# Kernel optimization log

Hardware: AMD Instinct MI355X
Metric: run time of the kernel (lower is better)

The kernel has to match this reference:

```python
import jax, jax.numpy as jnp
import numpy as np

NUM_HEADS = 6

def setup_inputs() -> dict:
    key = jax.random.key(0)
    k1, k2, k3, k4 = jax.random.split(key, 4)
    B, T, C = 128, 256, 384
    s = 1.0 / np.sqrt(C)
    return {
        'x': jax.random.normal(k1, (B, T, C), dtype=jnp.float32),
        'Wq': jax.random.normal(k2, (C, C), dtype=jnp.float32) * s,
        'Wk': jax.random.normal(k3, (C, C), dtype=jnp.float32) * s,
        'Wv': jax.random.normal(k4, (C, C), dtype=jnp.float32) * s,
    }

def reference(x, Wq, Wk, Wv):
    B, T, C = x.shape
    H = NUM_HEADS
    d = C // H
    # projections (bias-free Linear), split into heads
    q = (x @ Wq).reshape(B, T, H, d)
    k = (x @ Wk).reshape(B, T, H, d)
    v = (x @ Wv).reshape(B, T, H, d)
    # NOTE: original scales by 1/sqrt(C), not 1/sqrt(head_dim)
    scale = 1.0 / jnp.sqrt(jnp.asarray(C, dtype=x.dtype))
    att = jnp.einsum('bqhd,bkhd->bhqk', q, k) * scale  # [B,H,T,T]
    causal = jnp.tril(jnp.ones((T, T), dtype=bool))
    att = jnp.where(causal, att, -jnp.inf)
    att = jax.nn.softmax(att, axis=-1)
    # dropout is identity in eval/deterministic mode
    out = jnp.einsum('bhqk,bkhd->bqhd', att, v)  # [B,T,H,d]
    return out.reshape(B, T, C)
```

## Files before the change

### kernel.cpp

```cpp
#include <hip/hip_runtime.h>


typedef unsigned short u16;
typedef float f32x4 __attribute__((ext_vector_type(4)));
typedef short s16x8 __attribute__((ext_vector_type(8)));

static constexpr int BB = 128;
static constexpr int TT = 256;
static constexpr int CC = 384;
static constexpr int HH = 6;
static constexpr int DD = 64;
static constexpr int MM = BB * TT;

static constexpr size_t QOFF  = 0;
static constexpr size_t KOFF  = (size_t)MM * CC;
static constexpr size_t VOFF  = (size_t)2 * MM * CC;
static constexpr size_t WTOFF = (size_t)3 * MM * CC;
static constexpr size_t XOFF  = WTOFF + (size_t)3 * CC * CC;

static constexpr float CSC = 0.07362242194579907f;

__device__ __forceinline__ u16 f2bf(float f) {
  unsigned u = __float_as_uint(f);
  u += 0x7fffu + ((u >> 16) & 1u);
  return (u16)(u >> 16);
}

__global__ void xconv(const float* __restrict__ X, u16* __restrict__ ws) {
  size_t i = (size_t)(blockIdx.x * 256 + threadIdx.x) * 8;
  f32x4 a0 = *(const f32x4*)(X + i);
  f32x4 a1 = *(const f32x4*)(X + i + 4);
  s16x8 ab;
#pragma unroll
  for (int j = 0; j < 4; ++j) { ab[j] = (short)f2bf(a0[j]); ab[4 + j] = (short)f2bf(a1[j]); }
  *(s16x8*)(ws + XOFF + i) = ab;
}

__global__ void wtrans(const float* __restrict__ Wq, const float* __restrict__ Wk,
                       const float* __restrict__ Wv, u16* __restrict__ ws) {
  const float* W = (blockIdx.y == 0) ? Wq : (blockIdx.y == 1) ? Wk : Wv;
  const float sc = (blockIdx.y == 0) ? CSC : 1.0f;
  u16* WT = ws + WTOFF + (size_t)blockIdx.y * CC * CC;
  int i = blockIdx.x * 256 + threadIdx.x;
  int k = i / CC, n = i % CC;
  WT[(size_t)n * CC + k] = f2bf(W[i] * sc);
}

__global__ __launch_bounds__(256) void gemm_qkv(u16* __restrict__ ws) {
  const u16* Xbf = ws + XOFF;
  const u16* WT3 = ws + WTOFF;

  __shared__ u16 As[128][72];
  __shared__ u16 Bs[128][72];

  const int tid = threadIdx.x;
  const int lane = tid & 63;
  const int w = tid >> 6;
  const int quad = lane >> 4;
  const int col = lane & 15;
  const int m0 = blockIdx.x * 128;
  const int n0 = blockIdx.y * 128;
  const int z = blockIdx.y / 3;
  const int wm = (w >> 1) * 64;
  const int wn = (w & 1) * 64;

  f32x4 acc[4][4] = {};

  for (int kt = 0; kt < 6; ++kt) {
    if (kt) __syncthreads();
#pragma unroll
    for (int i = 0; i < 4; ++i) {
      int c = i * 256 + tid;
      int row = c >> 3, c8 = (c & 7) * 8;
      *(uint4*)(&As[row][c8]) =
          *(const uint4*)(Xbf + (size_t)(m0 + row) * CC + kt * 64 + c8);
      *(uint4*)(&Bs[row][c8]) =
          *(const uint4*)(WT3 + (size_t)(n0 + row) * CC + kt * 64 + c8);
    }
    __syncthreads();

    s16x8 af[4][2], bf[4][2];
#pragma unroll
    for (int mt = 0; mt < 4; ++mt)
#pragma unroll
      for (int ks = 0; ks < 2; ++ks)
        af[mt][ks] = *(const s16x8*)(&As[wm + mt * 16 + col][ks * 32 + quad * 8]);
#pragma unroll
    for (int nt = 0; nt < 4; ++nt)
#pragma unroll
      for (int ks = 0; ks < 2; ++ks)
        bf[nt][ks] = *(const s16x8*)(&Bs[wn + nt * 16 + col][ks * 32 + quad * 8]);

#pragma unroll
    for (int ks = 0; ks < 2; ++ks)
#pragma unroll
      for (int mt = 0; mt < 4; ++mt)
#pragma unroll
        for (int nt = 0; nt < 4; ++nt)
          acc[mt][nt] = __builtin_amdgcn_mfma_f32_16x16x32_bf16(
              af[mt][ks], bf[nt][ks], acc[mt][nt], 0, 0, 0);
  }

  if (z == 2) {
#pragma unroll
    for (int mt = 0; mt < 4; ++mt)
#pragma unroll
      for (int nt = 0; nt < 4; ++nt) {
        int tok = m0 + wm + mt * 16 + quad * 4;
        int bb = tok >> 8, t = tok & 255;
        int ng = (n0 - 2 * CC) + wn + nt * 16 + col;
        int hh = ng >> 6, d = ng & 63;
        uint2 pk;
        pk.x = (unsigned)f2bf(acc[mt][nt][0]) | ((unsigned)f2bf(acc[mt][nt][1]) << 16);
        pk.y = (unsigned)f2bf(acc[mt][nt][2]) | ((unsigned)f2bf(acc[mt][nt][3]) << 16);
        *(uint2*)(ws + VOFF + (((size_t)(bb * HH + hh) * DD + d) * TT + t)) = pk;
      }
  } else {
    u16* Y = ws + (size_t)z * MM * CC;
    const int nz = n0 - z * CC;
#pragma unroll
    for (int mt = 0; mt < 4; ++mt)
#pragma unroll
      for (int nt = 0; nt < 4; ++nt) {
        int mg = m0 + wm + mt * 16 + quad * 4;
        int ng = nz + wn + nt * 16 + col;
#pragma unroll
        for (int r = 0; r < 4; ++r)
          Y[(size_t)(mg + r) * CC + ng] = f2bf(acc[mt][nt][r]);
      }
  }
}

__global__ __launch_bounds__(128) void attn(const u16* __restrict__ ws,
                                            float* __restrict__ out) {
  const int bx = blockIdx.x;
  const int qt = 3 - (bx / 768);
  const int bh = bx % 768;
  const int b = bh / HH;
  const int h = bh % HH;

  __shared__ u16 Ps[2][16][72];

  const int tid = threadIdx.x;
  const int lane = tid & 63;
  const int w = tid >> 6;
  const int quad = lane >> 4;
  const int col = lane & 15;
  const int q0 = qt * 64 + w * 32;

  const u16* Qg = ws + QOFF;
  const u16* Kg = ws + KOFF;
  const u16* VTg = ws + VOFF;

  s16x8 qf[2][2];
#pragma unroll
  for (int mt = 0; mt < 2; ++mt)
#pragma unroll
    for (int ks = 0; ks < 2; ++ks)
      qf[mt][ks] = *(const s16x8*)(Qg + (size_t)(b * TT + q0 + mt * 16 + col) * CC +
                                   h * DD + ks * 32 + quad * 8);

  f32x4 o[2][4] = {};
  float mst[2] = {-1.0e30f, -1.0e30f}, lst[2] = {0.0f, 0.0f};

  for (int kt = 0; kt <= qt; ++kt) {
    s16x8 kf[4][2], vf[4][2];
#pragma unroll
    for (int nt = 0; nt < 4; ++nt)
#pragma unroll
      for (int ks = 0; ks < 2; ++ks) {
        kf[nt][ks] = *(const s16x8*)(Kg + (size_t)(b * TT + kt * 64 + nt * 16 + col) * CC +
                                     h * DD + ks * 32 + quad * 8);
        vf[nt][ks] = *(const s16x8*)(VTg + ((size_t)(bh * DD + nt * 16 + col) * TT +
                                     kt * 64 + ks * 32 + quad * 8));
      }

#pragma unroll
    for (int mt = 0; mt < 2; ++mt) {
      f32x4 s[4] = {};
#pragma unroll
      for (int ks = 0; ks < 2; ++ks)
#pragma unroll
        for (int nt = 0; nt < 4; ++nt)
          s[nt] = __builtin_amdgcn_mfma_f32_16x16x32_bf16(kf[nt][ks], qf[mt][ks],
                                                          s[nt], 0, 0, 0);

      float rmax = -1.0e30f;
#pragma unroll
      for (int nt = 0; nt < 4; ++nt)
#pragma unroll
        for (int r = 0; r < 4; ++r) {
          float t = s[nt][r];
          if (kt == qt && (nt * 16 + quad * 4 + r) > (w * 32 + mt * 16 + col)) t = -1.0e30f;
          s[nt][r] = t;
          rmax = fmaxf(rmax, t);
        }
      rmax = fmaxf(rmax, __shfl_xor(rmax, 16));
      rmax = fmaxf(rmax, __shfl_xor(rmax, 32));

      float mn = fmaxf(mst[mt], rmax);
      float alpha = exp2f(mst[mt] - mn);
      mst[mt] = mn;

      float lsum = 0.0f;
      unsigned pk[4][2];
#pragma unroll
      for (int nt = 0; nt < 4; ++nt) {
        float p0 = exp2f(s[nt][0] - mn), p1 = exp2f(s[nt][1] - mn);
        float p2 = exp2f(s[nt][2] - mn), p3 = exp2f(s[nt][3] - mn);
        lsum += (p0 + p1) + (p2 + p3);
        pk[nt][0] = (unsigned)f2bf(p0) | ((unsigned)f2bf(p1) << 16);
        pk[nt][1] = (unsigned)f2bf(p2) | ((unsigned)f2bf(p3) << 16);
      }
      lst[mt] = lst[mt] * alpha + lsum;

#pragma unroll
      for (int dt = 0; dt < 4; ++dt)
#pragma unroll
        for (int r = 0; r < 4; ++r) o[mt][dt][r] *= alpha;

      asm volatile("s_waitcnt lgkmcnt(0)" ::: "memory");
#pragma unroll
      for (int nt = 0; nt < 4; ++nt)
        *(uint2*)(&Ps[w][col][nt * 16 + quad * 4]) = make_uint2(pk[nt][0], pk[nt][1]);
      asm volatile("s_waitcnt lgkmcnt(0)" ::: "memory");

      s16x8 pf[2];
#pragma unroll
      for (int ks = 0; ks < 2; ++ks)
        pf[ks] = *(const s16x8*)(&Ps[w][col][ks * 32 + quad * 8]);

#pragma unroll
      for (int ks = 0; ks < 2; ++ks)
#pragma unroll
        for (int dt = 0; dt < 4; ++dt)
          o[mt][dt] = __builtin_amdgcn_mfma_f32_16x16x32_bf16(vf[dt][ks], pf[ks],
                                                              o[mt][dt], 0, 0, 0);
    }
  }

#pragma unroll
  for (int mt = 0; mt < 2; ++mt) {
    float l = lst[mt];
    l += __shfl_xor(l, 16);
    l += __shfl_xor(l, 32);
    float inv = 1.0f / l;
    int q = q0 + mt * 16 + col;
#pragma unroll
    for (int dt = 0; dt < 4; ++dt) {
      f32x4 res;
#pragma unroll
      for (int r = 0; r < 4; ++r) res[r] = o[mt][dt][r] * inv;
      *(f32x4*)(out + (size_t)(b * TT + q) * CC + h * DD + dt * 16 + quad * 4) = res;
    }
  }
}

extern "C" void kernel_launch(void* const* d_in, const int* in_sizes, int n_in,
                              void* d_out, int out_size, void* d_ws, size_t ws_size,
                              hipStream_t stream) {
  const float* x  = (const float*)d_in[0];
  const float* wq = (const float*)d_in[1];
  const float* wk = (const float*)d_in[2];
  const float* wv = (const float*)d_in[3];
  u16* ws  = (u16*)d_ws;
  float* out = (float*)d_out;

  xconv<<<dim3(MM * CC / (256 * 8)), 256, 0, stream>>>(x, ws);
  wtrans<<<dim3(CC * CC / 256, 3), 256, 0, stream>>>(wq, wk, wv, ws);
  gemm_qkv<<<dim3(MM / 128, 9), 256, 0, stream>>>(ws);
  attn<<<dim3(BB * HH * 4), 128, 0, stream>>>(ws, out);
}
```

Measured before the change: 184.0 us.

## Merge prep kernels and load GEMM tiles via direct global-to-LDS with XOR swizzle

Folds the x conversion and weight transpose kernels into a single prep launch to save one kernel launch. In the QKV GEMM, the tile staging now uses global_load_lds to copy straight from global memory into shared memory, skipping the register round trip. The unpadded LDS tiles use an XOR swizzle on 16-byte chunks to avoid bank conflicts. This depends on the lane-to-LDS address mapping of the builtin matching the swizzled layout.

After: 180.3 us. -2.0%, faster.

```diff
diff --git a/kernel.cpp b/kernel.cpp
--- a/kernel.cpp
+++ b/kernel.cpp
@@ -26,32 +26,42 @@
   return (u16)(u >> 16);
 }
 
-__global__ void xconv(const float* __restrict__ X, u16* __restrict__ ws) {
-  size_t i = (size_t)(blockIdx.x * 256 + threadIdx.x) * 8;
-  f32x4 a0 = *(const f32x4*)(X + i);
-  f32x4 a1 = *(const f32x4*)(X + i + 4);
-  s16x8 ab;
-#pragma unroll
-  for (int j = 0; j < 4; ++j) { ab[j] = (short)f2bf(a0[j]); ab[4 + j] = (short)f2bf(a1[j]); }
-  *(s16x8*)(ws + XOFF + i) = ab;
-}
-
-__global__ void wtrans(const float* __restrict__ Wq, const float* __restrict__ Wk,
-                       const float* __restrict__ Wv, u16* __restrict__ ws) {
-  const float* W = (blockIdx.y == 0) ? Wq : (blockIdx.y == 1) ? Wk : Wv;
-  const float sc = (blockIdx.y == 0) ? CSC : 1.0f;
-  u16* WT = ws + WTOFF + (size_t)blockIdx.y * CC * CC;
-  int i = blockIdx.x * 256 + threadIdx.x;
-  int k = i / CC, n = i % CC;
-  WT[(size_t)n * CC + k] = f2bf(W[i] * sc);
+__device__ __forceinline__ void g2l16(const u16* g, u16* l) {
+  __builtin_amdgcn_global_load_lds(
+      (const __attribute__((address_space(1))) u16*)g,
+      (__attribute__((address_space(3))) u16*)l, 16, 0, 0);
+}
+
+__global__ void prep(const float* __restrict__ X, const float* __restrict__ Wq,
+                     const float* __restrict__ Wk, const float* __restrict__ Wv,
+                     u16* __restrict__ ws) {
+  int bx = blockIdx.x;
+  if (bx < 6144) {
+    size_t i = (size_t)(bx * 256 + threadIdx.x) * 8;
+    f32x4 a0 = *(const f32x4*)(X + i);
+    f32x4 a1 = *(const f32x4*)(X + i + 4);
+    s16x8 ab;
+#pragma unroll
+    for (int j = 0; j < 4; ++j) { ab[j] = (short)f2bf(a0[j]); ab[4 + j] = (short)f2bf(a1[j]); }
+    *(s16x8*)(ws + XOFF + i) = ab;
+  } else {
+    int j = bx - 6144;
+    int z = j / 576;
+    const float* W = (z == 0) ? Wq : (z == 1) ? Wk : Wv;
+    const float sc = (z == 0) ? CSC : 1.0f;
+    u16* WT = ws + WTOFF + (size_t)z * CC * CC;
+    int i = (j % 576) * 256 + threadIdx.x;
+    int k = i / CC, n = i % CC;
+    WT[(size_t)n * CC + k] = f2bf(W[i] * sc);
+  }
 }
 
 __global__ __launch_bounds__(256) void gemm_qkv(u16* __restrict__ ws) {
   const u16* Xbf = ws + XOFF;
   const u16* WT3 = ws + WTOFF;
 
-  __shared__ u16 As[128][72];
-  __shared__ u16 Bs[128][72];
+  __shared__ u16 As[128][64];
+  __shared__ u16 Bs[128][64];
 
   const int tid = threadIdx.x;
   const int lane = tid & 63;
@@ -64,18 +74,18 @@
   const int wm = (w >> 1) * 64;
   const int wn = (w & 1) * 64;
 
+  const int rl = lane >> 3;
+  const int gb = (lane & 7) ^ rl;
+
   f32x4 acc[4][4] = {};
 
   for (int kt = 0; kt < 6; ++kt) {
     if (kt) __syncthreads();
 #pragma unroll
     for (int i = 0; i < 4; ++i) {
-      int c = i * 256 + tid;
-      int row = c >> 3, c8 = (c & 7) * 8;
-      *(uint4*)(&As[row][c8]) =
-          *(const uint4*)(Xbf + (size_t)(m0 + row) * CC + kt * 64 + c8);
-      *(uint4*)(&Bs[row][c8]) =
-          *(const uint4*)(WT3 + (size_t)(n0 + row) * CC + kt * 64 + c8);
+      int r0 = (w * 4 + i) * 8;
+      g2l16(Xbf + (size_t)(m0 + r0 + rl) * CC + kt * 64 + gb * 8, &As[r0][0]);
+      g2l16(WT3 + (size_t)(n0 + r0 + rl) * CC + kt * 64 + gb * 8, &Bs[r0][0]);
     }
     __syncthreads();
 
@@ -84,12 +94,14 @@
     for (int mt = 0; mt < 4; ++mt)
 #pragma unroll
       for (int ks = 0; ks < 2; ++ks)
-        af[mt][ks] = *(const s16x8*)(&As[wm + mt * 16 + col][ks * 32 + quad * 8]);
+        af[mt][ks] = *(const s16x8*)(&As[wm + mt * 16 + col]
+                                        [(((ks * 4 + quad) ^ (col & 7)) * 8)]);
 #pragma unroll
     for (int nt = 0; nt < 4; ++nt)
 #pragma unroll
       for (int ks = 0; ks < 2; ++ks)
-        bf[nt][ks] = *(const s16x8*)(&Bs[wn + nt * 16 + col][ks * 32 + quad * 8]);
+        bf[nt][ks] = *(const s16x8*)(&Bs[wn + nt * 16 + col]
+                                        [(((ks * 4 + quad) ^ (col & 7)) * 8)]);
 
 #pragma unroll
     for (int ks = 0; ks < 2; ++ks)
@@ -266,8 +278,7 @@
   u16* ws  = (u16*)d_ws;
   float* out = (float*)d_out;
 
-  xconv<<<dim3(MM * CC / (256 * 8)), 256, 0, stream>>>(x, ws);
-  wtrans<<<dim3(CC * CC / 256, 3), 256, 0, stream>>>(wq, wk, wv, ws);
+  prep<<<dim3(6144 + 1728), 256, 0, stream>>>(x, wq, wk, wv, ws);
   gemm_qkv<<<dim3(MM / 128, 9), 256, 0, stream>>>(ws);
   attn<<<dim3(BB * HH * 4), 128, 0, stream>>>(ws, out);
 }
```
